# Kernel optimization log

Hardware: AMD Instinct MI355X
Metric: run time of the kernel (lower is better)

The kernel has to match this reference:

```python
import jax, jax.numpy as jnp
import numpy as np

T_STEPS = 40        # 30 gated steps + 10 extra steps (original while<30 then for min(10,..))
GATED_STEPS = 30
BATCH = 4096
X_DIM = 150
H_DIM = 150


def setup_inputs() -> dict:
    key = jax.random.key(0)
    ks = jax.random.split(key, 11)
    s = lambda k, shape: jax.random.normal(k, shape, jnp.float32) * 0.05
    return {
        "x": jax.random.normal(ks[0], (T_STEPS, BATCH, X_DIM), jnp.float32),
        "w_ih": s(ks[1], (4 * H_DIM, X_DIM)),
        "w_hh": s(ks[2], (4 * H_DIM, H_DIM)),
        "b_ih": s(ks[3], (4 * H_DIM,)),
        "b_hh": s(ks[4], (4 * H_DIM,)),
        "w1": s(ks[5], (50, X_DIM + H_DIM)),
        "b1": s(ks[6], (50,)),
        "w2": s(ks[7], (25, 50)),
        "b2": s(ks[8], (25,)),
        "w3": s(ks[9], (2, 25)),
        "b3": s(ks[10], (2,)),
    }


def reference(x, w_ih, w_hh, b_ih, b_hh, w1, b1, w2, b2, w3, b3):
    B = x.shape[1]
    H = w_hh.shape[1]

    def cell(h, c, xt):
        # PyTorch LSTMCell: gate order i, f, g, o
        g = xt @ w_ih.T + b_ih + h @ w_hh.T + b_hh  # [B, 4H]
        i, f, gg, o = jnp.split(g, 4, axis=-1)
        c = jax.nn.sigmoid(f) * c + jax.nn.sigmoid(i) * jnp.tanh(gg)
        h = jax.nn.sigmoid(o) * jnp.tanh(c)
        return h, c

    def stop_gate(h, xt):
        # original detaches the concat input (requires_grad=False on .data)
        t = jax.lax.stop_gradient(jnp.concatenate([h, xt], axis=-1))  # [B, 300]
        t = jax.nn.relu(t @ w1.T + b1)
        t = jax.nn.relu(t @ w2.T + b2)
        return jax.nn.softmax(jax.nn.relu(t @ w3.T + b3), axis=-1)  # [B, 2]

    def step_gated(carry, xt):
        h, c = carry
        h, c = cell(h, c, xt)
        y = stop_gate(h, xt)
        return (h, c), (h, y)

    def step_plain(carry, xt):
        h, c = carry
        h, c = cell(h, c, xt)
        return (h, c), h

    h0 = jnp.zeros((B, H), x.dtype)
    c0 = jnp.zeros((B, H), x.dtype)
    (h, c), (hs1, ys) = jax.lax.scan(step_gated, (h0, c0), x[:GATED_STEPS])
    outh = h  # h_t at the end of the gated phase (original `outh`)
    (h, c), hs2 = jax.lax.scan(step_plain, (h, c), x[GATED_STEPS:])
    outputs = jnp.concatenate([hs1, hs2], axis=0)  # [T, B, H]
    return outh, outputs, ys
```

## Files before the change

### kernel.cpp

```cpp
#include <hip/hip_runtime.h>
#include <math.h>

#define TSTEPS 40
#define GATED  30
#define BATCH  4096
#define XD     150
#define HD     150
#define HP     160
#define PITCHW 328
#define SXP    328
#define WROWS  704
#define ROWS   16
#define NT     512
#define NBLK   (BATCH / ROWS)

#define TCH    4
#define S1P    66
#define S2P    27

#define OFF_OUTPUTS 614400
#define OFF_YS      25190400

typedef float  floatx4 __attribute__((ext_vector_type(4)));
typedef short  shortx8 __attribute__((ext_vector_type(8)));

__device__ __forceinline__ unsigned short bf16_rne(float f) {
    union { float f; unsigned int u; } v; v.f = f;
    unsigned int u = v.u;
    return (unsigned short)((u + 0x7fffu + ((u >> 16) & 1u)) >> 16);
}
__device__ __forceinline__ unsigned int pk2bf(float a, float b) {
    return (unsigned int)bf16_rne(a) | ((unsigned int)bf16_rne(b) << 16);
}
__device__ __forceinline__ float rcp_f(float x) {
    return __builtin_amdgcn_rcpf(x);
}
__device__ __forceinline__ float sigf(float x) {
    return rcp_f(1.0f + __expf(-x));
}
__device__ __forceinline__ float tanh_fast(float x) {
    x = fminf(fmaxf(x, -15.0f), 15.0f);
    float t = __expf(2.0f * x);
    return (t - 1.0f) * rcp_f(t + 1.0f);
}
__device__ __forceinline__ void bar_lds() {
    asm volatile("s_waitcnt lgkmcnt(0)\n\ts_barrier" ::: "memory");
}

__global__ void pack_weights(const float* __restrict__ w_ih, const float* __restrict__ w_hh,
                             const float* __restrict__ b_ih, const float* __restrict__ b_hh,
                             const float* __restrict__ w1,
                             unsigned short* __restrict__ Wc, float* __restrict__ bcp) {
    int idx = blockIdx.x * blockDim.x + threadIdx.x;
    int stride = gridDim.x * blockDim.x;
    for (int i = idx; i < WROWS * PITCHW; i += stride) {
        int j = i / PITCHW, k = i - j * PITCHW;
        float v = 0.0f;
        if (j < 640) {
            int tp = j / HP, u = j - tp * HP;
            if (u < 150) {
                int src = tp * 150 + u;
                if (k < 150)                    v = w_ih[src * 150 + k];
                else if (k >= 160 && k < 310)   v = w_hh[src * 150 + (k - 160)];
            }
        } else {
            int j1 = j - 640;
            if (j1 < 50) {
                if (k < 150)                    v = w1[j1 * 300 + 150 + k];
                else if (k >= 160 && k < 310)   v = w1[j1 * 300 + (k - 160)];
            }
        }
        Wc[i] = bf16_rne(v);
    }
    for (int i = idx; i < 640; i += stride) {
        int tp = i / HP, u = i - tp * HP;
        bcp[i] = (u < 150) ? (b_ih[tp * 150 + u] + b_hh[tp * 150 + u]) : 0.0f;
    }
}

__global__ __launch_bounds__(NT, 2)
void lstm_main(const float* __restrict__ x,
               const unsigned short* __restrict__ Wc,
               const float* __restrict__ bcp, const float* __restrict__ b1,
               const float* __restrict__ w2, const float* __restrict__ b2,
               const float* __restrict__ w3, const float* __restrict__ b3,
               float* __restrict__ outh, float* __restrict__ outputs,
               float* __restrict__ ys) {
    __shared__ unsigned short sxh[2][ROWS][SXP];
    __shared__ float sge[ROWS][4][33];
    __shared__ unsigned short wlds[8][16][SXP];
    __shared__ float bcs[640], b1s[64];
    __shared__ float sw2[1250], sb2[25], sw3[50], sb3[2];

    unsigned short (*stage4)[SXP] = (unsigned short(*)[SXP])&wlds[0][0][0];
    float (*st1p)[S1P] = (float(*)[S1P])((char*)&wlds[0][0][0] + 41984);
    float (*st2p)[S2P] = (float(*)[S2P])((char*)&wlds[0][0][0] + 58880);

    const int tid  = threadIdx.x;
    const int lane = tid & 63;
    const int wv   = tid >> 6;
    const int lrow = lane & 15;
    const int lq   = lane >> 4;
    const int row0 = blockIdx.x * ROWS;
    const int ty   = wv >> 1;
    const int ch   = wv & 1;

    for (int i = tid; i < 2 * ROWS * SXP; i += NT) {
        int b = i / (ROWS * SXP);
        int rem = i - b * (ROWS * SXP);
        int r = rem / SXP, k = rem - r * SXP;
        if (k >= 150) sxh[b][r][k] = 0;
    }
    for (int i = tid; i < ROWS * 75; i += NT) {
        int rr = i / 75, kk = i - rr * 75;
        float2 v = *(const float2*)(x + ((size_t)row0 + rr) * XD + 2 * kk);
        *(unsigned int*)&sxh[0][rr][2 * kk] = pk2bf(v.x, v.y);
    }
    for (int i = tid; i < 8 * 16 * 160; i += NT) {
        int w = i / (16 * 160);
        int rem = i - w * (16 * 160);
        int r = rem / 160, k = rem - r * 160;
        int et = 10 * (w >> 1) + 8 + (w & 1);
        *(unsigned int*)&wlds[w][r][2 * k] =
            *(const unsigned int*)&Wc[(size_t)(et * 16 + r) * PITCHW + 2 * k];
    }
    for (int i = tid; i < 640; i += NT) bcs[i] = bcp[i];
    if (tid < 64) b1s[tid] = (tid < 50) ? b1[tid] : 0.0f;
    for (int i = tid; i < 1250; i += NT) sw2[i] = w2[i];
    if (tid < 25) sb2[tid] = b2[tid];
    if (tid < 50) sw3[tid] = w3[tid];
    if (tid < 2)  sb3[tid] = b3[tid];

    shortx8 bfr[40];
#pragma unroll
    for (int j = 0; j < 4; ++j) {
        const unsigned short* wp =
            Wc + (size_t)((10 * j + wv) * 16 + lrow) * PITCHW + lq * 8;
#pragma unroll
        for (int kb = 0; kb < 10; ++kb)
            bfr[j * 10 + kb] = *(const shortx8*)(wp + kb * 32);
    }

    __syncthreads();

    const int uq = wv * 16 + lrow;
    const float bcq0 = bcs[uq];
    const float bcq1 = bcs[160 + uq];
    const float bcq2 = bcs[320 + uq];
    const float bcq3 = bcs[480 + uq];
    const int ce_c = tid & 31;
    const int ue = 128 + ce_c;
    const int re = tid >> 5;
    const float bce0 = bcs[ue];
    const float bce1 = bcs[160 + ue];
    const float bce2 = bcs[320 + ue];
    const float bce3 = bcs[480 + ue];
    const int pr0 = tid / 75,          pk0 = tid % 75;
    const int pr1 = (tid + 512) / 75,  pk1 = (tid + 512) % 75;
    const int pr2 = (tid + 1024) / 75, pk2 = (tid + 1024) % 75;

    float* outc = outputs + (size_t)(row0 + lq * 4) * HD + uq;
    float* oute = outputs + (size_t)(row0 + re) * HD + ue;

    float cr[4] = {0.f, 0.f, 0.f, 0.f};
    float cex = 0.f;

    unsigned short (*sxc)[SXP] = sxh[0];
    unsigned short (*sxn)[SXP] = sxh[1];

    for (int t = 0; t < TSTEPS; ++t) {
        float2 px0, px1, px2;
        const bool pf = (t + 1 < TSTEPS);
        if (pf) {
            const float* xn = x + ((size_t)(t + 1) * BATCH + row0) * XD;
            px0 = *(const float2*)(xn + pr0 * XD + 2 * pk0);
            px1 = *(const float2*)(xn + pr1 * XD + 2 * pk1);
            if (tid < 176) px2 = *(const float2*)(xn + pr2 * XD + 2 * pk2);
        }

        floatx4 acc[5];
#pragma unroll
        for (int j = 0; j < 5; ++j) acc[j] = (floatx4){0.f, 0.f, 0.f, 0.f};
#pragma unroll
        for (int kb = 0; kb < 10; ++kb) {
            shortx8 a = *(const shortx8*)&sxc[lrow][kb * 32 + lq * 8];
#pragma unroll
            for (int j = 0; j < 4; ++j)
                acc[j] = __builtin_amdgcn_mfma_f32_16x16x32_bf16(
                    a, bfr[j * 10 + kb], acc[j], 0, 0, 0);
            shortx8 b4 = *(const shortx8*)&wlds[wv][lrow][kb * 32 + lq * 8];
            acc[4] = __builtin_amdgcn_mfma_f32_16x16x32_bf16(a, b4, acc[4], 0, 0, 0);
        }
#pragma unroll
        for (int rg = 0; rg < 4; ++rg)
            sge[lq * 4 + rg][ty][ch * 16 + lrow] = acc[4][rg];

#pragma unroll
        for (int rg = 0; rg < 4; ++rg) {
            float gi = acc[0][rg] + bcq0;
            float gf = acc[1][rg] + bcq1;
            float gg = acc[2][rg] + bcq2;
            float go = acc[3][rg] + bcq3;
            float cn = sigf(gf) * cr[rg] + sigf(gi) * tanh_fast(gg);
            cr[rg] = cn;
            float h = sigf(go) * tanh_fast(cn);
            sxn[lq * 4 + rg][HP + uq] = bf16_rne(h);
            outc[rg * HD] = h;
            if (t == GATED - 1)
                outh[(size_t)(row0 + lq * 4 + rg) * HD + uq] = h;
        }
        if (pf) {
            *(unsigned int*)&sxn[pr0][2 * pk0] = pk2bf(px0.x, px0.y);
            *(unsigned int*)&sxn[pr1][2 * pk1] = pk2bf(px1.x, px1.y);
            if (tid < 176)
                *(unsigned int*)&sxn[pr2][2 * pk2] = pk2bf(px2.x, px2.y);
        }
        bar_lds();

        {
            float gi = sge[re][0][ce_c] + bce0;
            float gf = sge[re][1][ce_c] + bce1;
            float gg = sge[re][2][ce_c] + bce2;
            float go = sge[re][3][ce_c] + bce3;
            float cn = sigf(gf) * cex + sigf(gi) * tanh_fast(gg);
            cex = cn;
            float h = sigf(go) * tanh_fast(cn);
            sxn[re][HP + ue] = bf16_rne(h);
            if (ue < 150) {
                oute[0] = h;
                if (t == GATED - 1)
                    outh[(size_t)(row0 + re) * HD + ue] = h;
            }
        }
        bar_lds();

        { unsigned short (*tmp)[SXP] = sxc; sxc = sxn; sxn = tmp; }
        outc += (size_t)BATCH * HD;
        oute += (size_t)BATCH * HD;
    }

    for (int i = tid; i < TCH * 16 * SXP; i += NT)
        ((unsigned short*)stage4)[i] = 0;
    __syncthreads();

    for (int t0 = 0; t0 < GATED; t0 += TCH) {
        const int tcur = (GATED - t0 < TCH) ? (GATED - t0) : TCH;

        for (int i = tid; i < tcur * 16 * 75; i += NT) {
            int row = i / 75, kk = i - row * 75;
            int r = row & 15, tl = row >> 4;
            size_t base = ((size_t)(t0 + tl) * BATCH + row0 + r) * (size_t)XD;
            float2 xv = *(const float2*)(x + base + 2 * kk);
            float2 hv = *(const float2*)(outputs + base + 2 * kk);
            *(unsigned int*)&stage4[row][2 * kk]      = pk2bf(xv.x, xv.y);
            *(unsigned int*)&stage4[row][HP + 2 * kk] = pk2bf(hv.x, hv.y);
        }
        __syncthreads();

#pragma unroll
        for (int jj = 0; jj < 2; ++jj) {
            int job = wv * 2 + jj;
            int tl = job >> 2, ct = job & 3;
            if (tl < tcur) {
                const unsigned short* wp1 =
                    Wc + (size_t)(640 + ct * 16 + lrow) * PITCHW + lq * 8;
                floatx4 aw = {0.f, 0.f, 0.f, 0.f};
#pragma unroll
                for (int kb = 0; kb < 10; ++kb) {
                    shortx8 a = *(const shortx8*)&stage4[tl * 16 + lrow][kb * 32 + lq * 8];
                    shortx8 b = *(const shortx8*)(wp1 + kb * 32);
                    aw = __builtin_amdgcn_mfma_f32_16x16x32_bf16(a, b, aw, 0, 0, 0);
                }
#pragma unroll
                for (int rg = 0; rg < 4; ++rg)
                    st1p[tl * 16 + lq * 4 + rg][ct * 16 + lrow] = aw[rg];
            }
        }
        __syncthreads();

        for (int e = tid; e < tcur * 16 * 64; e += NT) {
            int s = e >> 6, j = e & 63;
            float v = st1p[s][j] + b1s[j];
            st1p[s][j] = v > 0.0f ? v : 0.0f;
        }
        __syncthreads();

        for (int u = tid; u < tcur * 16 * 25; u += NT) {
            int s = u / 25, j = u - s * 25;
            float a = sb2[j];
            const float* w2r = &sw2[j * 50];
#pragma unroll 10
            for (int k2 = 0; k2 < 50; ++k2)
                a = fmaf(w2r[k2], st1p[s][k2], a);
            st2p[s][j] = a > 0.0f ? a : 0.0f;
        }
        __syncthreads();

        if (tid < tcur * 16) {
            int tl = tid >> 4, r = tid & 15;
            float z0 = sb3[0], z1 = sb3[1];
#pragma unroll
            for (int k2 = 0; k2 < 25; ++k2) {
                z0 = fmaf(sw3[k2],      st2p[tid][k2], z0);
                z1 = fmaf(sw3[25 + k2], st2p[tid][k2], z1);
            }
            z0 = z0 > 0.0f ? z0 : 0.0f;
            z1 = z1 > 0.0f ? z1 : 0.0f;
            float mx = fmaxf(z0, z1);
            float e0 = __expf(z0 - mx), e1 = __expf(z1 - mx);
            float inv = 1.0f / (e0 + e1);
            size_t yb = ((size_t)(t0 + tl) * BATCH + row0 + r) * 2;
            ys[yb]     = e0 * inv;
            ys[yb + 1] = e1 * inv;
        }
        __syncthreads();
    }
}

extern "C" void kernel_launch(void* const* d_in, const int* in_sizes, int n_in,
                              void* d_out, int out_size, void* d_ws, size_t ws_size,
                              hipStream_t stream) {
    const float* x    = (const float*)d_in[0];
    const float* w_ih = (const float*)d_in[1];
    const float* w_hh = (const float*)d_in[2];
    const float* b_ih = (const float*)d_in[3];
    const float* b_hh = (const float*)d_in[4];
    const float* w1   = (const float*)d_in[5];
    const float* b1   = (const float*)d_in[6];
    const float* w2   = (const float*)d_in[7];
    const float* b2   = (const float*)d_in[8];
    const float* w3   = (const float*)d_in[9];
    const float* b3   = (const float*)d_in[10];

    float* out = (float*)d_out;
    unsigned short* Wc  = (unsigned short*)d_ws;
    float*          bcp = (float*)(Wc + WROWS * PITCHW);

    pack_weights<<<256, 256, 0, stream>>>(w_ih, w_hh, b_ih, b_hh, w1, Wc, bcp);

    lstm_main<<<NBLK, NT, 0, stream>>>(
        x, Wc, bcp, b1, w2, b2, w3, b3,
        out, out + OFF_OUTPUTS, out + OFF_YS);
}
```

Baseline: 318.9 us.

## Overlap extra-unit LSTM update with MFMA and move stop gate to separate kernel

The leftover-unit gate update (units 128-159) moves from a separate phase after a second barrier into the middle of the next step's MFMA loop. It is delayed by one step and its h is written into the current buffer before the last k-block is consumed. This removes one barrier per timestep. The stop-gate MLP is taken out of the recurrent kernel's tail and launched as its own fully parallel kernel over (timestep, 64-row tile) blocks. That frees LDS in the main kernel but re-reads x and outputs from global memory and adds a launch.

New measurement: 330.1 us. 1.04x slower.

```diff
diff --git a/kernel.cpp b/kernel.cpp
--- a/kernel.cpp
+++ b/kernel.cpp
@@ -14,7 +14,6 @@
 #define NT     512
 #define NBLK   (BATCH / ROWS)
 
-#define TCH    4
 #define S1P    66
 #define S2P    27
 
@@ -81,20 +80,12 @@
 __global__ __launch_bounds__(NT, 2)
 void lstm_main(const float* __restrict__ x,
                const unsigned short* __restrict__ Wc,
-               const float* __restrict__ bcp, const float* __restrict__ b1,
-               const float* __restrict__ w2, const float* __restrict__ b2,
-               const float* __restrict__ w3, const float* __restrict__ b3,
-               float* __restrict__ outh, float* __restrict__ outputs,
-               float* __restrict__ ys) {
+               const float* __restrict__ bcp,
+               float* __restrict__ outh, float* __restrict__ outputs) {
     __shared__ unsigned short sxh[2][ROWS][SXP];
     __shared__ float sge[ROWS][4][33];
     __shared__ unsigned short wlds[8][16][SXP];
-    __shared__ float bcs[640], b1s[64];
-    __shared__ float sw2[1250], sb2[25], sw3[50], sb3[2];
-
-    unsigned short (*stage4)[SXP] = (unsigned short(*)[SXP])&wlds[0][0][0];
-    float (*st1p)[S1P] = (float(*)[S1P])((char*)&wlds[0][0][0] + 41984);
-    float (*st2p)[S2P] = (float(*)[S2P])((char*)&wlds[0][0][0] + 58880);
+    __shared__ float bcs[640];
 
     const int tid  = threadIdx.x;
     const int lane = tid & 63;
@@ -125,11 +116,6 @@
             *(const unsigned int*)&Wc[(size_t)(et * 16 + r) * PITCHW + 2 * k];
     }
     for (int i = tid; i < 640; i += NT) bcs[i] = bcp[i];
-    if (tid < 64) b1s[tid] = (tid < 50) ? b1[tid] : 0.0f;
-    for (int i = tid; i < 1250; i += NT) sw2[i] = w2[i];
-    if (tid < 25) sb2[tid] = b2[tid];
-    if (tid < 50) sw3[tid] = w3[tid];
-    if (tid < 2)  sb3[tid] = b3[tid];
 
     shortx8 bfr[40];
 #pragma unroll
@@ -160,7 +146,6 @@
     const int pr2 = (tid + 1024) / 75, pk2 = (tid + 1024) % 75;
 
     float* outc = outputs + (size_t)(row0 + lq * 4) * HD + uq;
-    float* oute = outputs + (size_t)(row0 + re) * HD + ue;
 
     float cr[4] = {0.f, 0.f, 0.f, 0.f};
     float cex = 0.f;
@@ -178,11 +163,19 @@
             if (tid < 176) px2 = *(const float2*)(xn + pr2 * XD + 2 * pk2);
         }
 
+        float ge0, ge1, ge2, ge3;
+        if (t > 0) {
+            ge0 = sge[re][0][ce_c];
+            ge1 = sge[re][1][ce_c];
+            ge2 = sge[re][2][ce_c];
+            ge3 = sge[re][3][ce_c];
+        }
+
         floatx4 acc[5];
 #pragma unroll
         for (int j = 0; j < 5; ++j) acc[j] = (floatx4){0.f, 0.f, 0.f, 0.f};
 #pragma unroll
-        for (int kb = 0; kb < 10; ++kb) {
+        for (int kb = 0; kb < 9; ++kb) {
             shortx8 a = *(const shortx8*)&sxc[lrow][kb * 32 + lq * 8];
 #pragma unroll
             for (int j = 0; j < 4; ++j)
@@ -191,6 +184,34 @@
             shortx8 b4 = *(const shortx8*)&wlds[wv][lrow][kb * 32 + lq * 8];
             acc[4] = __builtin_amdgcn_mfma_f32_16x16x32_bf16(a, b4, acc[4], 0, 0, 0);
         }
+
+        if (t > 0) {
+            float gi = ge0 + bce0;
+            float gf = ge1 + bce1;
+            float gg = ge2 + bce2;
+            float go = ge3 + bce3;
+            float cn = sigf(gf) * cex + sigf(gi) * tanh_fast(gg);
+            cex = cn;
+            float h = sigf(go) * tanh_fast(cn);
+            sxc[re][HP + ue] = bf16_rne(h);
+            if (ue < 150) {
+                outputs[((size_t)(t - 1) * BATCH + row0 + re) * HD + ue] = h;
+                if (t == GATED)
+                    outh[(size_t)(row0 + re) * HD + ue] = h;
+            }
+        }
+        bar_lds();
+
+        {
+            shortx8 a = *(const shortx8*)&sxc[lrow][9 * 32 + lq * 8];
+#pragma unroll
+            for (int j = 0; j < 4; ++j)
+                acc[j] = __builtin_amdgcn_mfma_f32_16x16x32_bf16(
+                    a, bfr[j * 10 + 9], acc[j], 0, 0, 0);
+            shortx8 b4 = *(const shortx8*)&wlds[wv][lrow][9 * 32 + lq * 8];
+            acc[4] = __builtin_amdgcn_mfma_f32_16x16x32_bf16(a, b4, acc[4], 0, 0, 0);
+        }
+
 #pragma unroll
         for (int rg = 0; rg < 4; ++rg)
             sge[lq * 4 + rg][ty][ch * 16 + lrow] = acc[4][rg];
@@ -217,103 +238,111 @@
         }
         bar_lds();
 
-        {
-            float gi = sge[re][0][ce_c] + bce0;
-            float gf = sge[re][1][ce_c] + bce1;
-            float gg = sge[re][2][ce_c] + bce2;
-            float go = sge[re][3][ce_c] + bce3;
-            float cn = sigf(gf) * cex + sigf(gi) * tanh_fast(gg);
-            cex = cn;
-            float h = sigf(go) * tanh_fast(cn);
-            sxn[re][HP + ue] = bf16_rne(h);
-            if (ue < 150) {
-                oute[0] = h;
-                if (t == GATED - 1)
-                    outh[(size_t)(row0 + re) * HD + ue] = h;
-            }
-        }
-        bar_lds();
-
         { unsigned short (*tmp)[SXP] = sxc; sxc = sxn; sxn = tmp; }
         outc += (size_t)BATCH * HD;
-        oute += (size_t)BATCH * HD;
-    }
-
-    for (int i = tid; i < TCH * 16 * SXP; i += NT)
-        ((unsigned short*)stage4)[i] = 0;
-    __syncthreads();
-
-    for (int t0 = 0; t0 < GATED; t0 += TCH) {
-        const int tcur = (GATED - t0 < TCH) ? (GATED - t0) : TCH;
-
-        for (int i = tid; i < tcur * 16 * 75; i += NT) {
-            int row = i / 75, kk = i - row * 75;
-            int r = row & 15, tl = row >> 4;
-            size_t base = ((size_t)(t0 + tl) * BATCH + row0 + r) * (size_t)XD;
-            float2 xv = *(const float2*)(x + base + 2 * kk);
-            float2 hv = *(const float2*)(outputs + base + 2 * kk);
-            *(unsigned int*)&stage4[row][2 * kk]      = pk2bf(xv.x, xv.y);
-            *(unsigned int*)&stage4[row][HP + 2 * kk] = pk2bf(hv.x, hv.y);
-        }
-        __syncthreads();
-
-#pragma unroll
-        for (int jj = 0; jj < 2; ++jj) {
-            int job = wv * 2 + jj;
-            int tl = job >> 2, ct = job & 3;
-            if (tl < tcur) {
-                const unsigned short* wp1 =
-                    Wc + (size_t)(640 + ct * 16 + lrow) * PITCHW + lq * 8;
-                floatx4 aw = {0.f, 0.f, 0.f, 0.f};
-#pragma unroll
-                for (int kb = 0; kb < 10; ++kb) {
-                    shortx8 a = *(const shortx8*)&stage4[tl * 16 + lrow][kb * 32 + lq * 8];
-                    shortx8 b = *(const shortx8*)(wp1 + kb * 32);
-                    aw = __builtin_amdgcn_mfma_f32_16x16x32_bf16(a, b, aw, 0, 0, 0);
-                }
-#pragma unroll
-                for (int rg = 0; rg < 4; ++rg)
-                    st1p[tl * 16 + lq * 4 + rg][ct * 16 + lrow] = aw[rg];
-            }
-        }
-        __syncthreads();
-
-        for (int e = tid; e < tcur * 16 * 64; e += NT) {
-            int s = e >> 6, j = e & 63;
-            float v = st1p[s][j] + b1s[j];
-            st1p[s][j] = v > 0.0f ? v : 0.0f;
-        }
-        __syncthreads();
-
-        for (int u = tid; u < tcur * 16 * 25; u += NT) {
-            int s = u / 25, j = u - s * 25;
-            float a = sb2[j];
-            const float* w2r = &sw2[j * 50];
+    }
+
+    {
+        float gi = sge[re][0][ce_c] + bce0;
+        float gf = sge[re][1][ce_c] + bce1;
+        float gg = sge[re][2][ce_c] + bce2;
+        float go = sge[re][3][ce_c] + bce3;
+        float cn = sigf(gf) * cex + sigf(gi) * tanh_fast(gg);
+        float h = sigf(go) * tanh_fast(cn);
+        if (ue < 150)
+            outputs[((size_t)(TSTEPS - 1) * BATCH + row0 + re) * HD + ue] = h;
+    }
+}
+
+__global__ __launch_bounds__(256, 2)
+void stop_gate(const float* __restrict__ x,
+               const unsigned short* __restrict__ Wc,
+               const float* __restrict__ b1,
+               const float* __restrict__ w2, const float* __restrict__ b2,
+               const float* __restrict__ w3, const float* __restrict__ b3,
+               const float* __restrict__ outputs, float* __restrict__ ys) {
+    __shared__ unsigned short sA[64][SXP];
+    __shared__ float st1[64][S1P];
+    __shared__ float st2[64][S2P];
+    __shared__ float sw2[1250], sb2[25], sw3[50], sb3[2], b1s[64];
+
+    const int tid  = threadIdx.x;
+    const int lane = tid & 63;
+    const int wv   = tid >> 6;
+    const int lrow = lane & 15;
+    const int lq   = lane >> 4;
+    const int t    = blockIdx.x >> 6;
+    const int row0 = (blockIdx.x & 63) * 64;
+
+    for (int i = tid; i < 64 * (SXP / 2); i += 256)
+        ((unsigned int*)sA)[i] = 0;
+    for (int i = tid; i < 1250; i += 256) sw2[i] = w2[i];
+    if (tid < 25) sb2[tid] = b2[tid];
+    if (tid < 50) sw3[tid] = w3[tid];
+    if (tid < 2)  sb3[tid] = b3[tid];
+    if (tid < 64) b1s[tid] = (tid < 50) ? b1[tid] : 0.0f;
+    __syncthreads();
+
+    for (int i = tid; i < 64 * 75; i += 256) {
+        int row = i / 75, kk = i - row * 75;
+        size_t base = ((size_t)t * BATCH + row0 + row) * (size_t)XD;
+        float2 xv = *(const float2*)(x + base + 2 * kk);
+        float2 hv = *(const float2*)(outputs + base + 2 * kk);
+        *(unsigned int*)&sA[row][2 * kk]      = pk2bf(xv.x, xv.y);
+        *(unsigned int*)&sA[row][HP + 2 * kk] = pk2bf(hv.x, hv.y);
+    }
+    __syncthreads();
+
+#pragma unroll
+    for (int ct = 0; ct < 4; ++ct) {
+        const unsigned short* wp1 =
+            Wc + (size_t)(640 + ct * 16 + lrow) * PITCHW + lq * 8;
+        floatx4 aw = {0.f, 0.f, 0.f, 0.f};
+#pragma unroll
+        for (int kb = 0; kb < 10; ++kb) {
+            shortx8 a = *(const shortx8*)&sA[wv * 16 + lrow][kb * 32 + lq * 8];
+            shortx8 b = *(const shortx8*)(wp1 + kb * 32);
+            aw = __builtin_amdgcn_mfma_f32_16x16x32_bf16(a, b, aw, 0, 0, 0);
+        }
+#pragma unroll
+        for (int rg = 0; rg < 4; ++rg)
+            st1[wv * 16 + lq * 4 + rg][ct * 16 + lrow] = aw[rg];
+    }
+    __syncthreads();
+
+    for (int e = tid; e < 64 * 64; e += 256) {
+        int s = e >> 6, j = e & 63;
+        float v = st1[s][j] + b1s[j];
+        st1[s][j] = v > 0.0f ? v : 0.0f;
+    }
+    __syncthreads();
+
+    for (int u = tid; u < 64 * 25; u += 256) {
+        int s = u / 25, j = u - s * 25;
+        float a = sb2[j];
+        const float* w2r = &sw2[j * 50];
 #pragma unroll 10
-            for (int k2 = 0; k2 < 50; ++k2)
-                a = fmaf(w2r[k2], st1p[s][k2], a);
-            st2p[s][j] = a > 0.0f ? a : 0.0f;
-        }
-        __syncthreads();
-
-        if (tid < tcur * 16) {
-            int tl = tid >> 4, r = tid & 15;
-            float z0 = sb3[0], z1 = sb3[1];
-#pragma unroll
-            for (int k2 = 0; k2 < 25; ++k2) {
-                z0 = fmaf(sw3[k2],      st2p[tid][k2], z0);
-                z1 = fmaf(sw3[25 + k2], st2p[tid][k2], z1);
-            }
-            z0 = z0 > 0.0f ? z0 : 0.0f;
-            z1 = z1 > 0.0f ? z1 : 0.0f;
-            float mx = fmaxf(z0, z1);
-            float e0 = __expf(z0 - mx), e1 = __expf(z1 - mx);
-            float inv = 1.0f / (e0 + e1);
-            size_t yb = ((size_t)(t0 + tl) * BATCH + row0 + r) * 2;
-            ys[yb]     = e0 * inv;
-            ys[yb + 1] = e1 * inv;
-        }
-        __syncthreads();
+        for (int k2 = 0; k2 < 50; ++k2)
+            a = fmaf(w2r[k2], st1[s][k2], a);
+        st2[s][j] = a > 0.0f ? a : 0.0f;
+    }
+    __syncthreads();
+
+    if (tid < 64) {
+        float z0 = sb3[0], z1 = sb3[1];
+#pragma unroll
+        for (int k2 = 0; k2 < 25; ++k2) {
+            z0 = fmaf(sw3[k2],      st2[tid][k2], z0);
+            z1 = fmaf(sw3[25 + k2], st2[tid][k2], z1);
+        }
+        z0 = z0 > 0.0f ? z0 : 0.0f;
+        z1 = z1 > 0.0f ? z1 : 0.0f;
+        float mx = fmaxf(z0, z1);
+        float e0 = __expf(z0 - mx), e1 = __expf(z1 - mx);
+        float inv = 1.0f / (e0 + e1);
+        size_t yb = ((size_t)t * BATCH + row0 + tid) * 2;
+        ys[yb]     = e0 * inv;
+        ys[yb + 1] = e1 * inv;
     }
 }
 
@@ -339,6 +368,8 @@
     pack_weights<<<256, 256, 0, stream>>>(w_ih, w_hh, b_ih, b_hh, w1, Wc, bcp);
 
     lstm_main<<<NBLK, NT, 0, stream>>>(
-        x, Wc, bcp, b1, w2, b2, w3, b3,
-        out, out + OFF_OUTPUTS, out + OFF_YS);
-}
+        x, Wc, bcp, out, out + OFF_OUTPUTS);
+
+    stop_gate<<<GATED * 64, 256, 0, stream>>>(
+        x, Wc, b1, w2, b2, w3, b3, out + OFF_OUTPUTS, out + OFF_YS);
+}
```
